# Optimization experiments

Measured on AMD Instinct MI355X. Metric: run time of the kernel, lower is better.

Reference implementation:

```python
import jax, jax.numpy as jnp
import numpy as np
import math

EMBED_DIM = 256
SEQ_LEN = 4096
BATCH = 4
NUM_SCALES = (24.0, 720.0)


def setup_inputs() -> dict:
    key = jax.random.key(0)
    ks = jax.random.split(key, 8)
    d = EMBED_DIM
    x = jax.random.normal(ks[0], (BATCH, SEQ_LEN, d), dtype=jnp.float32)
    # nn.Linear params: weight [out, in], bias [out]
    s = 1.0 / math.sqrt(d)
    Wq = jax.random.uniform(ks[1], (d, d), jnp.float32, -s, s)
    bq = jax.random.uniform(ks[2], (d,), jnp.float32, -s, s)
    Wk = jax.random.uniform(ks[3], (d, d), jnp.float32, -s, s)
    bk = jax.random.uniform(ks[4], (d,), jnp.float32, -s, s)
    Wv = jax.random.uniform(ks[5], (d, d), jnp.float32, -s, s)
    bv = jax.random.uniform(ks[6], (d,), jnp.float32, -s, s)
    beta = jnp.ones((len(NUM_SCALES),), dtype=jnp.float32)
    return {"x": x, "Wq": Wq, "bq": bq, "Wk": Wk, "bk": bk, "Wv": Wv, "bv": bv, "beta": beta}


def reference(x, Wq, bq, Wk, bk, Wv, bv, beta):
    d = x.shape[-1]
    seq_len = x.shape[1]
    sqrt_d = jnp.asarray(math.sqrt(d), x.dtype)
    # Linear: y = x @ W^T + b
    Q = jnp.einsum('bsd,ed->bse', x, Wq) + bq
    K = jnp.einsum('bsd,ed->bse', x, Wk) + bk
    V = jnp.einsum('bsd,ed->bse', x, Wv) + bv
    attn = jnp.einsum('bse,bte->bst', Q, K) / sqrt_d  # [B,S,S]
    # multi-scale periodic bias (batch-independent): sum_n beta[n]*cos(2*pi*|i-j|/T_n)
    idx = jnp.arange(seq_len, dtype=jnp.float32)
    absdiff = jnp.abs(idx[:, None] - idx[None, :])  # [S,S]
    two_pi = jnp.asarray(2.0 * math.pi, jnp.float32)
    bias = jnp.zeros((seq_len, seq_len), dtype=jnp.float32)
    for n, T in enumerate(NUM_SCALES):
        bias = bias + beta[n] * jnp.cos(two_pi * absdiff / T)
    scores = jax.nn.softmax(attn + bias[None, :, :], axis=-1)
    return jnp.einsum('bst,bte->bse', scores, V)
```

## Files before the change

### kernel.cpp

```cpp
#include <hip/hip_runtime.h>
#include <math.h>
#include <stdint.h>

#define DEV static __device__ __forceinline__
typedef unsigned short u16;

constexpr int D = 256;
constexpr int S = 4096;
constexpr int QSTR = 272;
constexpr int KT_TILE = 8960;
constexpr int VT_TILE = 10240;

typedef short bf16x8 __attribute__((ext_vector_type(8)));
typedef float f32x16 __attribute__((ext_vector_type(16)));

DEV u16 f2bf(float f){ __bf16 b = (__bf16)f; return __builtin_bit_cast(u16, b); }
DEV float bf2f(u16 h){ return __uint_as_float(((unsigned)h)<<16); }
DEV int packbf(float lo, float hi){ return (int)((((unsigned)f2bf(hi)) << 16) | (unsigned)f2bf(lo)); }
DEV float bfsum2(int d){
  return __uint_as_float(((unsigned)d)<<16) + __uint_as_float(((unsigned)d) & 0xffff0000u);
}
DEV void gl_lds16(const u16* g, u16* l) {
  __builtin_amdgcn_global_load_lds(
      (const __attribute__((address_space(1))) unsigned int*)g,
      (__attribute__((address_space(3))) unsigned int*)l, 16, 0, 0);
}

DEV void softmax_pf(const f32x16& s, int h, float& l_acc, bf16x8* pf) {
  #pragma unroll
  for (int s2 = 0; s2 < 2; ++s2) {
    float e0 = __expf(s[8*s2+0]), e1 = __expf(s[8*s2+1]);
    float e2 = __expf(s[8*s2+2]), e3 = __expf(s[8*s2+3]);
    float e4 = __expf(s[8*s2+4]), e5 = __expf(s[8*s2+5]);
    float e6 = __expf(s[8*s2+6]), e7 = __expf(s[8*s2+7]);
    int P0d0 = packbf(e0, e1), P0d1 = packbf(e2, e3);
    int P1d0 = packbf(e4, e5), P1d1 = packbf(e6, e7);
    l_acc += bfsum2(P0d0) + bfsum2(P0d1) + bfsum2(P1d0) + bfsum2(P1d1);
    int s0 = h ? P0d0 : P1d0;
    int s1 = h ? P0d1 : P1d1;
    int r0 = __shfl_xor(s0, 32, 64);
    int r1 = __shfl_xor(s1, 32, 64);
    union { int d[4]; bf16x8 v; } u;
    u.d[0] = h ? r0 : P0d0;
    u.d[1] = h ? r1 : P0d1;
    u.d[2] = h ? P1d0 : r0;
    u.d[3] = h ? P1d1 : r1;
    pf[s2] = u.v;
  }
}

__global__ __launch_bounds__(256) void msp_prep(
    const float* __restrict__ x, const float* __restrict__ Wq,
    const float* __restrict__ Wk, const float* __restrict__ Wv,
    const float* __restrict__ beta,
    u16* __restrict__ xc, u16* __restrict__ Wc,
    u16* __restrict__ Qb, u16* __restrict__ Kt,
    float* __restrict__ Lacc)
{
  const int blk = blockIdx.x, tid = threadIdx.x;
  if (blk < 2048) {
    int row = blk*8 + (tid>>5);
    int col = (tid&31)*8;
    const float* p = x + (size_t)row*256 + col;
    union { u16 s[8]; uint4 v; } hh, ll;
    #pragma unroll
    for (int i=0;i<8;++i){ float v = p[i]; u16 h2 = f2bf(v); hh.s[i]=h2; ll.s[i]=f2bf(v - bf2f(h2)); }
    *(uint4*)(xc + (size_t)row*512 + col)       = hh.v;
    *(uint4*)(xc + (size_t)row*512 + 256 + col) = ll.v;
  } else if (blk < 2144) {
    int q = blk - 2048;
    int mat = q >> 5;
    int idx = (q & 31)*2048 + tid*8;
    int o = idx >> 8, cc = idx & 255;
    const float* W = mat==0 ? Wq : (mat==1 ? Wk : Wv);
    float sc = (mat==0) ? 0.0625f : 1.0f;
    const float* p = W + (size_t)o*256 + cc;
    union { u16 s[8]; uint4 v; } hh, ll;
    #pragma unroll
    for (int i=0;i<8;++i){ float v = p[i]*sc; u16 h2 = f2bf(v); hh.s[i]=h2; ll.s[i]=f2bf(v - bf2f(h2)); }
    *(uint4*)(Wc + (size_t)(mat*256 + o)*512 + cc)       = hh.v;
    *(uint4*)(Wc + (size_t)(mat*256 + o)*512 + 256 + cc) = ll.v;
  } else if (blk < 2208) {
    int row = (blk - 2144)*256 + tid;
    int s = row & (S-1);
    int bb = row >> 12;
    float b0 = beta[0], b1 = beta[1];
    int i24 = s % 24, i720 = s % 720;
    float t0 = (float)i24  * 0.26179938779914944f;
    float t1 = (float)i720 * 0.008726646259971648f;
    float c0 = cosf(t0), s0 = sinf(t0), c1 = cosf(t1), s1 = sinf(t1);
    float qv[4] = {b0*c0, b0*s0, b1*c1, b1*s1};
    float kv[4] = {c0, s0, c1, s1};
    u16* qp = Qb + (size_t)row*QSTR + 256;
    u16* kp = Kt + (size_t)(bb*128 + (s>>5))*KT_TILE + (s&31)*280 + 256;
    #pragma unroll
    for (int n=0;n<4;++n){
      u16 uh = f2bf(qv[n]); u16 ul = f2bf(qv[n]-bf2f(uh));
      u16 vh = f2bf(kv[n]); u16 vl = f2bf(kv[n]-bf2f(vh));
      qp[n*3+0]=uh; qp[n*3+1]=uh; qp[n*3+2]=ul;
      kp[n*3+0]=vh; kp[n*3+1]=vl; kp[n*3+2]=vh;
    }
    #pragma unroll
    for (int c=12;c<16;++c){ qp[c]=0; kp[c]=0; }
  } else {
    float4* p = (float4*)Lacc;
    float4 z = {0.f,0.f,0.f,0.f};
    #pragma unroll
    for (int c=0;c<16;++c) p[tid + c*256] = z;
  }
}

__global__ __launch_bounds__(256, 2) void msp_proj(
    const u16* __restrict__ xc, const u16* __restrict__ Wc,
    const float* __restrict__ bq, const float* __restrict__ bk, const float* __restrict__ bv,
    u16* __restrict__ Qb, u16* __restrict__ Kt, u16* __restrict__ Vt)
{
  __shared__ __align__(16) u16 smem[2][2][128][72];

  const int tid = threadIdx.x;
  const int w = tid >> 6, lane = tid & 63;
  const int l31 = lane & 31, h = lane >> 5;
  const int m0 = blockIdx.x * 128;
  const int nblk = blockIdx.y;
  const int n0 = nblk * 128, mat = nblk >> 1, cb = (nblk & 1) * 128;
  const int mh = (w & 1) * 64, nh = (w >> 1) * 64;

  const int srow = tid & 127;
  const int isB = tid >> 7;
  const u16* sgbase = isB ? (Wc + (size_t)(n0 + srow)*512) : (xc + (size_t)(m0 + srow)*512);

  {
    u16* d = &smem[0][isB][srow][0];
    #pragma unroll
    for (int jj=0; jj<8; ++jj) *(uint4*)(d + jj*8) = *(const uint4*)(sgbase + jj*8);
  }

  f32x16 acc[2][2];
  #pragma unroll
  for (int a=0;a<2;++a)
    #pragma unroll
    for (int c=0;c<2;++c)
      #pragma unroll
      for (int i=0;i<16;++i) acc[a][c][i] = 0.f;

  for (int kc8 = 0; kc8 < 8; ++kc8) {
    __syncthreads();
    const int p = kc8 & 1;
    uint4 nxt[8];
    if (kc8 < 7) {
      const u16* g = sgbase + (kc8+1)*64;
      #pragma unroll
      for (int jj=0; jj<8; ++jj) nxt[jj] = *(const uint4*)(g + jj*8);
    }
    #pragma unroll
    for (int kf = 0; kf < 4; ++kf) {
      const int ko = kf*16 + h*8;
      bf16x8 a0 = *(const bf16x8*)&smem[p][0][mh + l31][ko];
      bf16x8 a1 = *(const bf16x8*)&smem[p][0][mh + 32 + l31][ko];
      bf16x8 b0 = *(const bf16x8*)&smem[p][1][nh + l31][ko];
      bf16x8 b1 = *(const bf16x8*)&smem[p][1][nh + 32 + l31][ko];
      acc[0][0] = __builtin_amdgcn_mfma_f32_32x32x16_bf16(a0, b0, acc[0][0], 0,0,0);
      acc[0][1] = __builtin_amdgcn_mfma_f32_32x32x16_bf16(a0, b1, acc[0][1], 0,0,0);
      acc[1][0] = __builtin_amdgcn_mfma_f32_32x32x16_bf16(a1, b0, acc[1][0], 0,0,0);
      acc[1][1] = __builtin_amdgcn_mfma_f32_32x32x16_bf16(a1, b1, acc[1][1], 0,0,0);
    }
    if (kc8 < 7) {
      u16* d = &smem[p^1][isB][srow][0];
      #pragma unroll
      for (int jj=0; jj<8; ++jj) *(uint4*)(d + jj*8) = nxt[jj];
    }
  }

  const float* bias = mat==0 ? bq : (mat==1 ? bk : bv);
  const float bsc = (mat==0) ? 0.0625f : 1.0f;
  float bb_[2];
  #pragma unroll
  for (int ntl=0; ntl<2; ++ntl) bb_[ntl] = bias[cb + nh + ntl*32 + l31] * bsc;

  if (mat <= 1) {
    #pragma unroll
    for (int mt=0; mt<2; ++mt)
      #pragma unroll
      for (int ntl=0; ntl<2; ++ntl)
        #pragma unroll
        for (int r=0; r<16; ++r) {
          int gm = m0 + mh + mt*32 + (r&3) + 8*(r>>2) + 4*h;
          int col = cb + nh + ntl*32 + l31;
          u16 val = f2bf(acc[mt][ntl][r] + bb_[ntl]);
          if (mat == 0) {
            Qb[(size_t)gm*QSTR + col] = val;
          } else {
            int bb2 = gm >> 12, s = gm & (S-1);
            Kt[(size_t)(bb2*128 + (s>>5))*KT_TILE + (s&31)*280 + col] = val;
          }
        }
  } else {
    u16* T = (u16*)smem;
    #pragma unroll
    for (int mt=0; mt<2; ++mt)
      #pragma unroll
      for (int ntl=0; ntl<2; ++ntl)
        #pragma unroll
        for (int r=0; r<16; ++r) {
          int e_loc = nh + ntl*32 + l31;
          int m_loc = mh + mt*32 + (r&3) + 8*(r>>2) + 4*h;
          T[(size_t)e_loc*136 + m_loc] = f2bf(acc[mt][ntl][r] + bb_[ntl]);
        }
    __syncthreads();
    int e_loc = tid >> 1, shalf = (tid & 1)*64;
    int e = cb + e_loc;
    #pragma unroll
    for (int g2 = 0; g2 < 2; ++g2) {
      int gm = m0 + shalf + g2*32;
      int bb2 = gm >> 12, s = gm & (S-1);
      u16* dst = Vt + (size_t)(bb2*128 + (s>>5))*VT_TILE + (size_t)e*40;
      const u16* src = T + (size_t)e_loc*136 + shalf + g2*32;
      #pragma unroll
      for (int k2=0;k2<4;++k2) *(uint4*)(dst + k2*8) = *(const uint4*)(src + k2*8);
    }
  }
}

__global__ __launch_bounds__(256, 2) void msp_attn(
    const u16* __restrict__ Qb, const u16* __restrict__ Kt,
    const u16* __restrict__ Vt, float* __restrict__ out,
    float* __restrict__ P1, float* __restrict__ P23,
    float* __restrict__ Lacc)
{
  __shared__ __align__(16) unsigned char smem[77824];

  const int tid = threadIdx.x;
  const int w = tid >> 6, lane = tid & 63;
  const int l31 = lane & 31, h = lane >> 5;

  const int xg = blockIdx.x;
  const int xcd = xg & 7, j = xg >> 3;
  const int c = xcd*2 + (j & 1);
  const int qt = j >> 1;
  const int b = c >> 2, tq = c & 3;
  const int q0 = qt * 128;
  const int qw = q0 + w*32;

  bf16x8 qf[17];
  {
    const u16* qp = Qb + ((size_t)b*S + qw + l31)*QSTR + h*8;
    #pragma unroll
    for (int s2=0; s2<17; ++s2) qf[s2] = *(const bf16x8*)(qp + s2*16);
  }

  const int tIdx0 = b*128 + tq*32;

  f32x16 oacc[8];
  #pragma unroll
  for (int e=0;e<8;++e)
    #pragma unroll
    for (int i=0;i<16;++i) oacc[e][i] = 0.f;
  float l_acc = 0.f;

  {
    const u16* kg = Kt + (size_t)tIdx0*KT_TILE;
    u16* kl = (u16*)smem;
    #pragma unroll
    for (int i = w; i < 18; i += 4) gl_lds16(kg + i*512 + lane*8, kl + i*512);
  }

  f32x16 sc_prev;

  {
    __syncthreads();
    const u16* kg = Kt + (size_t)(tIdx0 + 1)*KT_TILE;
    u16* kl = (u16*)(smem + 18432);
    #pragma unroll
    for (int i = w; i < 18; i += 4) gl_lds16(kg + i*512 + lane*8, kl + i*512);
    const u16* vg = Vt + (size_t)tIdx0*VT_TILE;
    u16* vl = (u16*)(smem + 36864);
    #pragma unroll
    for (int i = w; i < 20; i += 4) gl_lds16(vg + i*512 + lane*8, vl + i*512);

    const u16* Kp = (const u16*)smem + (size_t)l31*280 + h*8;
    f32x16 sa;
    #pragma unroll
    for (int i=0;i<16;++i) sa[i] = 0.f;
    __builtin_amdgcn_s_setprio(1);
    #pragma unroll
    for (int s2 = 0; s2 < 17; ++s2) {
      bf16x8 kf = *(const bf16x8*)(Kp + s2*16);
      sa = __builtin_amdgcn_mfma_f32_32x32x16_bf16(kf, qf[s2], sa, 0,0,0);
    }
    __builtin_amdgcn_s_setprio(0);
    sc_prev = sa;
  }

  for (int it = 1; it < 32; ++it) {
    const int p = it & 1;
    __syncthreads();

    if (it < 31) {
      const u16* kg = Kt + (size_t)(tIdx0 + it + 1)*KT_TILE;
      u16* kl = (u16*)(smem + (p^1)*18432);
      #pragma unroll
      for (int i = w; i < 18; i += 4) gl_lds16(kg + i*512 + lane*8, kl + i*512);
    }
    {
      const u16* vg = Vt + (size_t)(tIdx0 + it)*VT_TILE;
      u16* vl = (u16*)(smem + 36864 + p*20480);
      #pragma unroll
      for (int i = w; i < 20; i += 4) gl_lds16(vg + i*512 + lane*8, vl + i*512);
    }

    bf16x8 pf[2];
    softmax_pf(sc_prev, h, l_acc, pf);

    const u16* Kp = (const u16*)(smem + p*18432) + (size_t)l31*280 + h*8;
    const u16* Vp = (const u16*)(smem + 36864 + (p^1)*20480) + (size_t)l31*40 + h*8;
    f32x16 sa;
    #pragma unroll
    for (int i=0;i<16;++i) sa[i] = 0.f;
    __builtin_amdgcn_s_setprio(1);
    #pragma unroll
    for (int s2 = 0; s2 < 17; ++s2) {
      bf16x8 kf = *(const bf16x8*)(Kp + s2*16);
      sa = __builtin_amdgcn_mfma_f32_32x32x16_bf16(kf, qf[s2], sa, 0,0,0);
      if (s2 < 16) {
        const u16* vb = Vp + (s2>>1)*(32*40) + (s2&1)*16;
        oacc[s2>>1] = __builtin_amdgcn_mfma_f32_32x32x16_bf16(*(const bf16x8*)vb, pf[s2&1], oacc[s2>>1], 0,0,0);
      }
    }
    __builtin_amdgcn_s_setprio(0);
    sc_prev = sa;
  }

  bf16x8 pf[2];
  softmax_pf(sc_prev, h, l_acc, pf);

  float l_tot = l_acc + __shfl_xor(l_acc, 32, 64);
  if (h == 0) unsafeAtomicAdd(&Lacc[(size_t)b*S + qw + l31], l_tot);

  __syncthreads();
  {
    const u16* Vp = (const u16*)(smem + 36864 + 20480) + (size_t)l31*40 + h*8;
    __builtin_amdgcn_s_setprio(1);
    #pragma unroll
    for (int et = 0; et < 8; ++et) {
      const u16* vb = Vp + et*32*40;
      oacc[et] = __builtin_amdgcn_mfma_f32_32x32x16_bf16(*(const bf16x8*)(vb),      pf[0], oacc[et], 0,0,0);
      oacc[et] = __builtin_amdgcn_mfma_f32_32x32x16_bf16(*(const bf16x8*)(vb + 16), pf[1], oacc[et], 0,0,0);
    }
    __builtin_amdgcn_s_setprio(0);
  }

  float* dst = (tq == 0) ? (out + (size_t)b*S*D)
             : (tq == 1) ? (P1 + (size_t)b*S*D)
                         : (P23 + ((size_t)(tq-2)*4 + b)*S*D);
  float* OflA = (float*)smem;
  float* OflB = (float*)smem + 8320;
  for (int rr = 0; rr < 2; ++rr) {
    __syncthreads();
    if ((w >> 1) == rr) {
      float* Of = (w & 1) ? OflB : OflA;
      #pragma unroll
      for (int et=0; et<8; ++et)
        #pragma unroll
        for (int g=0; g<4; ++g) {
          float4 v4 = { oacc[et][4*g+0], oacc[et][4*g+1], oacc[et][4*g+2], oacc[et][4*g+3] };
          *(float4*)&Of[(size_t)l31*260 + et*32 + 8*g + 4*h] = v4;
        }
    }
    __syncthreads();
    #pragma unroll
    for (int hf = 0; hf < 2; ++hf) {
      const float* Of = hf ? OflB : OflA;
      float* obase = dst + (size_t)(q0 + (rr*2 + hf)*32)*D;
      #pragma unroll
      for (int q2 = 0; q2 < 8; ++q2) {
        int q = q2*4 + (tid>>6);
        int e4 = (tid & 63)*4;
        *(float4*)(obase + (size_t)q*D + e4) = *(const float4*)&Of[(size_t)q*260 + e4];
      }
    }
  }
}

__global__ __launch_bounds__(256) void msp_norm(
    float* __restrict__ out, const float* __restrict__ P1,
    const float* __restrict__ P23, const float* __restrict__ L)
{
  constexpr size_t PSZ = (size_t)4*S*D;
  int idx = blockIdx.x*256 + threadIdx.x;
  int row = idx >> 6, e0 = (idx & 63)*4;
  size_t off = (size_t)row*256 + e0;
  float inv = 1.0f / L[row];
  float4 v  = *(const float4*)(out + off);
  float4 a  = *(const float4*)(P1  + off);
  float4 b2 = *(const float4*)(P23 + off);
  float4 c2 = *(const float4*)(P23 + PSZ + off);
  v.x = (v.x + a.x + b2.x + c2.x) * inv;
  v.y = (v.y + a.y + b2.y + c2.y) * inv;
  v.z = (v.z + a.z + b2.z + c2.z) * inv;
  v.w = (v.w + a.w + b2.w + c2.w) * inv;
  *(float4*)(out + off) = v;
}

extern "C" void kernel_launch(void* const* d_in, const int* in_sizes, int n_in,
                              void* d_out, int out_size, void* d_ws, size_t ws_size,
                              hipStream_t stream) {
  const float* x    = (const float*)d_in[0];
  const float* Wq   = (const float*)d_in[1];
  const float* bq   = (const float*)d_in[2];
  const float* Wk   = (const float*)d_in[3];
  const float* bk   = (const float*)d_in[4];
  const float* Wv   = (const float*)d_in[5];
  const float* bv   = (const float*)d_in[6];
  const float* beta = (const float*)d_in[7];
  float* out = (float*)d_out;

  char* w = (char*)d_ws;
  u16* xc = (u16*)w;
  float* P1 = (float*)w;
  w += (size_t)16384*512*2;
  u16* Wc = (u16*)w;  w += (size_t)768*512*2;
  u16* Qb = (u16*)w;  w += (size_t)16384*QSTR*2;
  u16* Kt = (u16*)w;  w += (size_t)512*KT_TILE*2;
  u16* Vt = (u16*)w;  w += (size_t)512*VT_TILE*2;
  float* Lacc = (float*)w; w += (size_t)16384*4;
  float* P23 = (float*)w;

  msp_prep<<<2209, 256, 0, stream>>>(x, Wq, Wk, Wv, beta, xc, Wc, Qb, Kt, Lacc);
  msp_proj<<<dim3(128, 6), 256, 0, stream>>>(xc, Wc, bq, bk, bv, Qb, Kt, Vt);
  msp_attn<<<512, 256, 0, stream>>>(Qb, Kt, Vt, out, P1, P23, Lacc);
  msp_norm<<<4096, 256, 0, stream>>>(out, P1, P23, Lacc);
}
```

Before: 208.0 us.

## Load V fragments directly to registers, fold log2e into Q scale, split QK accumulators

V tiles are no longer staged through LDS. Each lane reads its V fragments straight from global memory into registers, one tile ahead, using a compact 32-element row stride, and the PV MFMAs run as a separate block after softmax. LDS use falls to 36 KB, and the output staging goes from two buffers to one buffer written in four rounds. The softmax uses exp2, with log2(e) folded into the Q weight/bias scale and the beta terms. The QK chain is split across two accumulators to shorten the MFMA dependency chain. The cost is more register pressure and global-load latency exposed in the loop.

```diff
diff --git a/kernel.cpp b/kernel.cpp
--- a/kernel.cpp
+++ b/kernel.cpp
@@ -9,7 +9,7 @@
 constexpr int S = 4096;
 constexpr int QSTR = 272;
 constexpr int KT_TILE = 8960;
-constexpr int VT_TILE = 10240;
+constexpr int VT_TILE = 8192;
 
 typedef short bf16x8 __attribute__((ext_vector_type(8)));
 typedef float f32x16 __attribute__((ext_vector_type(16)));
@@ -20,6 +20,7 @@
 DEV float bfsum2(int d){
   return __uint_as_float(((unsigned)d)<<16) + __uint_as_float(((unsigned)d) & 0xffff0000u);
 }
+DEV float ex2(float x){ return __builtin_amdgcn_exp2f(x); }
 DEV void gl_lds16(const u16* g, u16* l) {
   __builtin_amdgcn_global_load_lds(
       (const __attribute__((address_space(1))) unsigned int*)g,
@@ -29,10 +30,10 @@
 DEV void softmax_pf(const f32x16& s, int h, float& l_acc, bf16x8* pf) {
   #pragma unroll
   for (int s2 = 0; s2 < 2; ++s2) {
-    float e0 = __expf(s[8*s2+0]), e1 = __expf(s[8*s2+1]);
-    float e2 = __expf(s[8*s2+2]), e3 = __expf(s[8*s2+3]);
-    float e4 = __expf(s[8*s2+4]), e5 = __expf(s[8*s2+5]);
-    float e6 = __expf(s[8*s2+6]), e7 = __expf(s[8*s2+7]);
+    float e0 = ex2(s[8*s2+0]), e1 = ex2(s[8*s2+1]);
+    float e2 = ex2(s[8*s2+2]), e3 = ex2(s[8*s2+3]);
+    float e4 = ex2(s[8*s2+4]), e5 = ex2(s[8*s2+5]);
+    float e6 = ex2(s[8*s2+6]), e7 = ex2(s[8*s2+7]);
     int P0d0 = packbf(e0, e1), P0d1 = packbf(e2, e3);
     int P1d0 = packbf(e4, e5), P1d1 = packbf(e6, e7);
     l_acc += bfsum2(P0d0) + bfsum2(P0d1) + bfsum2(P1d0) + bfsum2(P1d1);
@@ -73,7 +74,7 @@
     int idx = (q & 31)*2048 + tid*8;
     int o = idx >> 8, cc = idx & 255;
     const float* W = mat==0 ? Wq : (mat==1 ? Wk : Wv);
-    float sc = (mat==0) ? 0.0625f : 1.0f;
+    float sc = (mat==0) ? 0.09016844005556021f : 1.0f;
     const float* p = W + (size_t)o*256 + cc;
     union { u16 s[8]; uint4 v; } hh, ll;
     #pragma unroll
@@ -84,7 +85,8 @@
     int row = (blk - 2144)*256 + tid;
     int s = row & (S-1);
     int bb = row >> 12;
-    float b0 = beta[0], b1 = beta[1];
+    constexpr float L2E = 1.4426950408889634f;
+    float b0 = beta[0]*L2E, b1 = beta[1]*L2E;
     int i24 = s % 24, i720 = s % 720;
     float t0 = (float)i24  * 0.26179938779914944f;
     float t1 = (float)i720 * 0.008726646259971648f;
@@ -172,7 +174,7 @@
   }
 
   const float* bias = mat==0 ? bq : (mat==1 ? bk : bv);
-  const float bsc = (mat==0) ? 0.0625f : 1.0f;
+  const float bsc = (mat==0) ? 0.09016844005556021f : 1.0f;
   float bb_[2];
   #pragma unroll
   for (int ntl=0; ntl<2; ++ntl) bb_[ntl] = bias[cb + nh + ntl*32 + l31] * bsc;
@@ -213,7 +215,7 @@
     for (int g2 = 0; g2 < 2; ++g2) {
       int gm = m0 + shalf + g2*32;
       int bb2 = gm >> 12, s = gm & (S-1);
-      u16* dst = Vt + (size_t)(bb2*128 + (s>>5))*VT_TILE + (size_t)e*40;
+      u16* dst = Vt + (size_t)(bb2*128 + (s>>5))*VT_TILE + (size_t)e*32;
       const u16* src = T + (size_t)e_loc*136 + shalf + g2*32;
       #pragma unroll
       for (int k2=0;k2<4;++k2) *(uint4*)(dst + k2*8) = *(const uint4*)(src + k2*8);
@@ -227,7 +229,7 @@
     float* __restrict__ P1, float* __restrict__ P23,
     float* __restrict__ Lacc)
 {
-  __shared__ __align__(16) unsigned char smem[77824];
+  __shared__ __align__(16) unsigned char smem[36864];
 
   const int tid = threadIdx.x;
   const int w = tid >> 6, lane = tid & 63;
@@ -257,6 +259,9 @@
     for (int i=0;i<16;++i) oacc[e][i] = 0.f;
   float l_acc = 0.f;
 
+  bf16x8 vf[8][2];
+  const u16* vbase = Vt + (size_t)l31*32 + h*8;
+
   {
     const u16* kg = Kt + (size_t)tIdx0*KT_TILE;
     u16* kl = (u16*)smem;
@@ -272,23 +277,27 @@
     u16* kl = (u16*)(smem + 18432);
     #pragma unroll
     for (int i = w; i < 18; i += 4) gl_lds16(kg + i*512 + lane*8, kl + i*512);
-    const u16* vg = Vt + (size_t)tIdx0*VT_TILE;
-    u16* vl = (u16*)(smem + 36864);
-    #pragma unroll
-    for (int i = w; i < 20; i += 4) gl_lds16(vg + i*512 + lane*8, vl + i*512);
+
+    const u16* vg = vbase + (size_t)tIdx0*VT_TILE;
+    #pragma unroll
+    for (int et=0; et<8; ++et)
+      #pragma unroll
+      for (int ks=0; ks<2; ++ks)
+        vf[et][ks] = *(const bf16x8*)(vg + et*1024 + ks*16);
 
     const u16* Kp = (const u16*)smem + (size_t)l31*280 + h*8;
-    f32x16 sa;
-    #pragma unroll
-    for (int i=0;i<16;++i) sa[i] = 0.f;
+    f32x16 sa, sb;
+    #pragma unroll
+    for (int i=0;i<16;++i){ sa[i] = 0.f; sb[i] = 0.f; }
     __builtin_amdgcn_s_setprio(1);
     #pragma unroll
     for (int s2 = 0; s2 < 17; ++s2) {
       bf16x8 kf = *(const bf16x8*)(Kp + s2*16);
-      sa = __builtin_amdgcn_mfma_f32_32x32x16_bf16(kf, qf[s2], sa, 0,0,0);
+      if (s2 & 1) sb = __builtin_amdgcn_mfma_f32_32x32x16_bf16(kf, qf[s2], sb, 0,0,0);
+      else        sa = __builtin_amdgcn_mfma_f32_32x32x16_bf16(kf, qf[s2], sa, 0,0,0);
     }
     __builtin_amdgcn_s_setprio(0);
-    sc_prev = sa;
+    sc_prev = sa + sb;
   }
 
   for (int it = 1; it < 32; ++it) {
@@ -301,33 +310,40 @@
       #pragma unroll
       for (int i = w; i < 18; i += 4) gl_lds16(kg + i*512 + lane*8, kl + i*512);
     }
-    {
-      const u16* vg = Vt + (size_t)(tIdx0 + it)*VT_TILE;
-      u16* vl = (u16*)(smem + 36864 + p*20480);
-      #pragma unroll
-      for (int i = w; i < 20; i += 4) gl_lds16(vg + i*512 + lane*8, vl + i*512);
-    }
 
     bf16x8 pf[2];
     softmax_pf(sc_prev, h, l_acc, pf);
 
+    __builtin_amdgcn_s_setprio(1);
+    #pragma unroll
+    for (int et = 0; et < 8; ++et) {
+      oacc[et] = __builtin_amdgcn_mfma_f32_32x32x16_bf16(vf[et][0], pf[0], oacc[et], 0,0,0);
+      oacc[et] = __builtin_amdgcn_mfma_f32_32x32x16_bf16(vf[et][1], pf[1], oacc[et], 0,0,0);
+    }
+    __builtin_amdgcn_s_setprio(0);
+
+    {
+      const u16* vg = vbase + (size_t)(tIdx0 + it)*VT_TILE;
+      #pragma unroll
+      for (int et=0; et<8; ++et)
+        #pragma unroll
+        for (int ks=0; ks<2; ++ks)
+          vf[et][ks] = *(const bf16x8*)(vg + et*1024 + ks*16);
+    }
+
     const u16* Kp = (const u16*)(smem + p*18432) + (size_t)l31*280 + h*8;
-    const u16* Vp = (const u16*)(smem + 36864 + (p^1)*20480) + (size_t)l31*40 + h*8;
-    f32x16 sa;
-    #pragma unroll
-    for (int i=0;i<16;++i) sa[i] = 0.f;
+    f32x16 sa, sb;
+    #pragma unroll
+    for (int i=0;i<16;++i){ sa[i] = 0.f; sb[i] = 0.f; }
     __builtin_amdgcn_s_setprio(1);
     #pragma unroll
     for (int s2 = 0; s2 < 17; ++s2) {
       bf16x8 kf = *(const bf16x8*)(Kp + s2*16);
-      sa = __builtin_amdgcn_mfma_f32_32x32x16_bf16(kf, qf[s2], sa, 0,0,0);
-      if (s2 < 16) {
-        const u16* vb = Vp + (s2>>1)*(32*40) + (s2&1)*16;
-        oacc[s2>>1] = __builtin_amdgcn_mfma_f32_32x32x16_bf16(*(const bf16x8*)vb, pf[s2&1], oacc[s2>>1], 0,0,0);
-      }
+      if (s2 & 1) sb = __builtin_amdgcn_mfma_f32_32x32x16_bf16(kf, qf[s2], sb, 0,0,0);
+      else        sa = __builtin_amdgcn_mfma_f32_32x32x16_bf16(kf, qf[s2], sa, 0,0,0);
     }
     __builtin_amdgcn_s_setprio(0);
-    sc_prev = sa;
+    sc_prev = sa + sb;
   }
 
   bf16x8 pf[2];
@@ -336,47 +352,36 @@
   float l_tot = l_acc + __shfl_xor(l_acc, 32, 64);
   if (h == 0) unsafeAtomicAdd(&Lacc[(size_t)b*S + qw + l31], l_tot);
 
-  __syncthreads();
-  {
-    const u16* Vp = (const u16*)(smem + 36864 + 20480) + (size_t)l31*40 + h*8;
-    __builtin_amdgcn_s_setprio(1);
-    #pragma unroll
-    for (int et = 0; et < 8; ++et) {
-      const u16* vb = Vp + et*32*40;
-      oacc[et] = __builtin_amdgcn_mfma_f32_32x32x16_bf16(*(const bf16x8*)(vb),      pf[0], oacc[et], 0,0,0);
-      oacc[et] = __builtin_amdgcn_mfma_f32_32x32x16_bf16(*(const bf16x8*)(vb + 16), pf[1], oacc[et], 0,0,0);
-    }
-    __builtin_amdgcn_s_setprio(0);
-  }
+  __builtin_amdgcn_s_setprio(1);
+  #pragma unroll
+  for (int et = 0; et < 8; ++et) {
+    oacc[et] = __builtin_amdgcn_mfma_f32_32x32x16_bf16(vf[et][0], pf[0], oacc[et], 0,0,0);
+    oacc[et] = __builtin_amdgcn_mfma_f32_32x32x16_bf16(vf[et][1], pf[1], oacc[et], 0,0,0);
+  }
+  __builtin_amdgcn_s_setprio(0);
 
   float* dst = (tq == 0) ? (out + (size_t)b*S*D)
              : (tq == 1) ? (P1 + (size_t)b*S*D)
                          : (P23 + ((size_t)(tq-2)*4 + b)*S*D);
-  float* OflA = (float*)smem;
-  float* OflB = (float*)smem + 8320;
-  for (int rr = 0; rr < 2; ++rr) {
-    __syncthreads();
-    if ((w >> 1) == rr) {
-      float* Of = (w & 1) ? OflB : OflA;
+  float* Ofl = (float*)smem;
+  for (int rnd = 0; rnd < 4; ++rnd) {
+    __syncthreads();
+    if (w == rnd) {
       #pragma unroll
       for (int et=0; et<8; ++et)
         #pragma unroll
         for (int g=0; g<4; ++g) {
           float4 v4 = { oacc[et][4*g+0], oacc[et][4*g+1], oacc[et][4*g+2], oacc[et][4*g+3] };
-          *(float4*)&Of[(size_t)l31*260 + et*32 + 8*g + 4*h] = v4;
+          *(float4*)&Ofl[(size_t)l31*260 + et*32 + 8*g + 4*h] = v4;
         }
     }
     __syncthreads();
-    #pragma unroll
-    for (int hf = 0; hf < 2; ++hf) {
-      const float* Of = hf ? OflB : OflA;
-      float* obase = dst + (size_t)(q0 + (rr*2 + hf)*32)*D;
-      #pragma unroll
-      for (int q2 = 0; q2 < 8; ++q2) {
-        int q = q2*4 + (tid>>6);
-        int e4 = (tid & 63)*4;
-        *(float4*)(obase + (size_t)q*D + e4) = *(const float4*)&Of[(size_t)q*260 + e4];
-      }
+    float* obase = dst + (size_t)(q0 + rnd*32)*D;
+    #pragma unroll
+    for (int q2 = 0; q2 < 8; ++q2) {
+      int q = q2*4 + (tid>>6);
+      int e4 = (tid & 63)*4;
+      *(float4*)(obase + (size_t)q*D + e4) = *(const float4*)&Ofl[(size_t)q*260 + e4];
     }
   }
 }
```

Result: slower. 390.1 us (+87.6%).
